# Kernel tuning notes

Hardware: AMD Instinct MI355X
Metric: run time of the kernel (lower is better)

Reference implementation:

```python
import jax, jax.numpy as jnp
import numpy as np

N_NODES = 50000
NEG_SLOPE = 0.2


def setup_inputs() -> dict:
    key = jax.random.key(0)
    ks = jax.random.split(key, 10)
    d = {
        'x': jax.random.normal(ks[0], (N_NODES, 128), dtype=jnp.float32),
        'edge_index': jax.random.randint(ks[1], (2, 800000), 0, N_NODES, dtype=jnp.int64),
        'W1': jax.random.normal(ks[2], (128, 512), dtype=jnp.float32) * (1.0 / np.sqrt(128)),
        'att_src1': jax.random.normal(ks[3], (8, 64), dtype=jnp.float32) * 0.1,
        'att_dst1': jax.random.normal(ks[4], (8, 64), dtype=jnp.float32) * 0.1,
        'b1': jax.random.normal(ks[5], (512,), dtype=jnp.float32) * 0.02,
        'W2': jax.random.normal(ks[6], (512, 1), dtype=jnp.float32) * (1.0 / np.sqrt(512)),
        'att_src2': jax.random.normal(ks[7], (1, 1), dtype=jnp.float32) * 0.1,
        'att_dst2': jax.random.normal(ks[8], (1, 1), dtype=jnp.float32) * 0.1,
        'b2': jax.random.normal(ks[9], (1,), dtype=jnp.float32) * 0.02,
    }
    return d


def _gat_layer(x, src, dst, W, a_src, a_dst, b):
    # x: [N, F_in]; W: [F_in, H*C]; a_src/a_dst: [H, C]; b: [H*C]
    N = x.shape[0]
    H, C = a_src.shape
    xh = (x @ W).reshape(N, H, C)                      # [N, H, C]
    s = jnp.sum(xh * a_src, axis=-1)                   # [N, H] source logits
    t = jnp.sum(xh * a_dst, axis=-1)                   # [N, H] target logits
    e = s[src] + t[dst]                                # [E, H]
    e = jnp.where(e > 0, e, NEG_SLOPE * e)             # leaky_relu(0.2)
    emax = jax.ops.segment_max(e, dst, num_segments=N)  # per-target max (self-loops guarantee coverage)
    ex = jnp.exp(e - emax[dst])                        # [E, H]
    denom = jax.ops.segment_sum(ex, dst, num_segments=N)  # [N, H]
    alpha = ex / denom[dst]                            # softmax over incoming edges
    msg = xh[src] * alpha[:, :, None]                  # [E, H, C]
    out = jax.ops.segment_sum(msg, dst, num_segments=N)   # [N, H, C]
    return out.reshape(N, H * C) + b


def reference(x, edge_index, W1, att_src1, att_dst1, b1, W2, att_src2, att_dst2, b2):
    N = x.shape[0]
    # add self-loops (PyG GATConv default)
    loop = jnp.arange(N, dtype=edge_index.dtype)
    src = jnp.concatenate([edge_index[0], loop])
    dst = jnp.concatenate([edge_index[1], loop])
    h = _gat_layer(x, src, dst, W1, att_src1, att_dst1, b1)   # [N, 512]
    h = jax.nn.relu(h)
    out = _gat_layer(h, src, dst, W2, att_src2, att_dst2, b2)  # [N, 1]
    return out.reshape(-1)
```

## Files before the change

### kernel.cpp

```cpp
#include <hip/hip_runtime.h>
#include <math.h>

#define NEG_SLOPE 0.2f

typedef __attribute__((ext_vector_type(8))) short bf16x8;
typedef __attribute__((ext_vector_type(4))) float f32x4;

__device__ __forceinline__ float leaky(float v){ return v > 0.f ? v : NEG_SLOPE * v; }

static __device__ __forceinline__ unsigned int f2bf(float x){
  unsigned u = __float_as_uint(x);
  return (u + 0x7fffu + ((u >> 16) & 1u)) >> 16;
}

__global__ __launch_bounds__(256) void k_prep0(
    const float* __restrict__ W1, const float* __restrict__ as, const float* __restrict__ ad,
    float* __restrict__ wst, bf16x8* __restrict__ packh,
    const int* __restrict__ dstp, int* __restrict__ deg8, int* __restrict__ erk,
    int N, int E)
{
  int b = blockIdx.x, tid = threadIdx.x;
  if (b == 0){
    for (int idx = tid; idx < 2048; idx += 256){
      int k = idx >> 4, o = idx & 15, half = o >> 3, hh = o & 7;
      const float* a = half ? ad : as;
      const float* wrow = W1 + (size_t)k * 512 + hh * 64;
      float sum = 0.f;
      for (int c = 0; c < 64; ++c) sum += wrow[c] * a[hh * 64 + c];
      wst[idx] = sum;
    }
  } else if (b < 33){
    int g = (b - 1) * 256 + tid;
    int gl = g & 63, kt = (g >> 6) & 3, ctl = (g >> 8) & 3, hh = g >> 10;
    int gc = hh * 64 + ctl * 16 + (gl & 15);
    int k0 = kt * 32 + (gl >> 4) * 8;
    bf16x8 hv;
    #pragma unroll
    for (int i = 0; i < 8; ++i)
      hv[i] = (short)f2bf(W1[(size_t)(k0 + i) * 512 + gc]);
    packh[g] = hv;
  } else {
    int i = (b - 33) * 256 + tid;
    if (i < E){
      int d = dstp[i];
      int s = b & 7;
      erk[i] = atomicAdd(&deg8[(size_t)s * N + d], 1);
    }
  }
}

__global__ __launch_bounds__(256) void k_scanlog(
    const int* __restrict__ deg8, int* __restrict__ sbase,
    int* __restrict__ tmp, int* __restrict__ bsum,
    const float* __restrict__ x, const float* __restrict__ wst,
    float* __restrict__ s, float* __restrict__ t, unsigned int* __restrict__ xb,
    int N, int nb)
{
  __shared__ float xs[64][133];
  __shared__ float wl[2048];
  __shared__ int ws4[4];
  int tid = threadIdx.x;
  int b = blockIdx.x;

  if (b < nb){
    int i = b * 256 + tid;
    int total = 0;
    if (i < N){
      int run = 0;
      #pragma unroll
      for (int sh = 0; sh < 8; ++sh){
        sbase[(size_t)sh * N + i] = run;
        run += deg8[(size_t)sh * N + i];
      }
      total = run;
    }
    int lane = tid & 63, wv = tid >> 6;
    int xv = total;
    #pragma unroll
    for (int off = 1; off < 64; off <<= 1){
      int y = __shfl_up(xv, off, 64);
      if (lane >= off) xv += y;
    }
    if (lane == 63) ws4[wv] = xv;
    __syncthreads();
    int p = 0;
    for (int w = 0; w < wv; ++w) p += ws4[w];
    xv += p;
    if (i < N) tmp[i] = xv;
    if (tid == 255) bsum[b] = xv;
  } else {
    int n0 = (b - nb) * 64;
    for (int i = tid; i < 2048; i += 256) wl[i] = wst[i];
    for (int i = tid; i < 2048; i += 256){
      int r = i >> 5, c4 = (i & 31) << 2;
      float4 v = make_float4(0.f, 0.f, 0.f, 0.f);
      if (n0 + r < N) v = *(const float4*)(x + (size_t)(n0 + r) * 128 + c4);
      xs[r][c4 + 0] = v.x; xs[r][c4 + 1] = v.y; xs[r][c4 + 2] = v.z; xs[r][c4 + 3] = v.w;
    }
    __syncthreads();
    int node = tid & 63, og = tid >> 6;
    int o = og * 4;
    float a0 = 0.f, a1 = 0.f, a2 = 0.f, a3 = 0.f;
    for (int k = 0; k < 128; ++k){
      float v = xs[node][k];
      float4 wv4 = *(const float4*)&wl[k * 16 + o];
      a0 += v * wv4.x;
      a1 += v * wv4.y;
      a2 += v * wv4.z;
      a3 += v * wv4.w;
    }
    int n = n0 + node;
    if (n < N){
      if (o < 8){
        s[n * 8 + o + 0] = a0; s[n * 8 + o + 1] = a1;
        s[n * 8 + o + 2] = a2; s[n * 8 + o + 3] = a3;
      } else {
        int oo = o - 8;
        t[n * 8 + oo + 0] = a0; t[n * 8 + oo + 1] = a1;
        t[n * 8 + oo + 2] = a2; t[n * 8 + oo + 3] = a3;
      }
    }
    for (int i = tid; i < 4096; i += 256){
      int r = i >> 6, j = i & 63;
      int n2 = n0 + r;
      if (n2 < N)
        xb[(size_t)n2 * 64 + j] = f2bf(xs[r][2 * j]) | (f2bf(xs[r][2 * j + 1]) << 16);
    }
  }
}

__global__ __launch_bounds__(256) void k_fill3(const int* __restrict__ src,
                        const int* __restrict__ dst, int E,
                        const int* __restrict__ tmp, const int* __restrict__ bsumraw,
                        const int* __restrict__ erk, const int* __restrict__ sbase,
                        int* __restrict__ rowptr, int* __restrict__ esrc, int N, int nb){
  __shared__ int bs[256];
  __shared__ int ws[4];
  int tid = threadIdx.x;
  {
    int v = (tid < nb) ? bsumraw[tid] : 0;
    int lane = tid & 63, wv = tid >> 6;
    int x = v;
    #pragma unroll
    for (int off = 1; off < 64; off <<= 1){
      int y = __shfl_up(x, off, 64);
      if (lane >= off) x += y;
    }
    if (lane == 63) ws[wv] = x;
    __syncthreads();
    int p = 0;
    for (int w = 0; w < wv; ++w) p += ws[w];
    bs[tid] = x + p;
    __syncthreads();
  }
  int i = blockIdx.x * 256 + tid;
  if (i <= N){
    int r;
    if (i == 0) r = 0;
    else { int ii = i - 1, blk = ii >> 8; r = tmp[ii] + (blk ? bs[blk - 1] : 0); }
    rowptr[i] = r;
  }
  if (i < E){
    int d = dst[i];
    int ii = d - 1, blk = ii >> 8;
    int row0 = (d == 0) ? 0 : tmp[ii] + (blk ? bs[blk - 1] : 0);
    int s = (33 + (i >> 8)) & 7;
    esrc[row0 + sbase[(size_t)s * N + d] + erk[i]] = src[i];
  }
}

__global__ __launch_bounds__(512, 8) void k_agg_gemm(
    const unsigned int* __restrict__ xb,
    const float* __restrict__ s, const float* __restrict__ t,
    const int* __restrict__ rowptr, const int* __restrict__ esrc,
    const bf16x8* __restrict__ packh,
    const float* __restrict__ b1, const float* __restrict__ W2,
    float* __restrict__ xh2, int N)
{
  __shared__ unsigned int ylds[8192];
  __shared__ float lal[8][128];
  __shared__ float red[8][16];
  int tid = threadIdx.x;
  int w = tid >> 6, lane = tid & 63;
  int m0 = blockIdx.x * 16;
  int h = lane & 7;
  int es = lane >> 3;

  for (int ni = 0; ni < 2; ++ni){
    int nl = w * 2 + ni;
    int n = m0 + nl;
    float acc[16];
    #pragma unroll
    for (int i = 0; i < 16; ++i) acc[i] = 0.f;

    if (n < N){
      int row0 = rowptr[n], deg = rowptr[n + 1] - row0;
      float tn = t[(unsigned)(n * 8 + h)];
      float sn = s[(unsigned)(n * 8 + h)];
      float selfe = __expf(leaky(sn + tn));

      {
        unsigned int v = xb[(unsigned)(n * 64 + lane)];
        float f0 = __uint_as_float(v << 16);
        float f1 = __uint_as_float(v & 0xffff0000u);
        #pragma unroll
        for (int hh = 0; hh < 8; ++hh){
          float a = __shfl(selfe, hh, 64);
          acc[2 * hh]     += a * f0;
          acc[2 * hh + 1] += a * f1;
        }
      }
      float dsum = (lane < 8) ? selfe : 0.f;

      float* lb = lal[w];
      for (int base = 0; base < deg; base += 8){
        float* la = lb + ((base >> 3) & 1) * 64;
        int e = base + es;
        int cnt = min(8, deg - base);
        int srcl = 0;
        if (e < deg) srcl = esrc[row0 + e];
        float sv = s[(unsigned)(srcl * 8 + h)];
        int sj[8];
        #pragma unroll
        for (int j = 0; j < 8; ++j) sj[j] = __shfl(srcl, j << 3, 64);
        unsigned int vv[8];
        #pragma unroll
        for (int j = 0; j < 8; ++j) vv[j] = xb[(unsigned)(sj[j] * 64 + lane)];
        float ev = (e < deg) ? __expf(leaky(sv + tn)) : 0.f;
        dsum += ev;
        la[lane] = ev;
        #pragma unroll
        for (int j = 0; j < 8; ++j){
          if (j < cnt){
            float4 q0 = *(float4*)&la[j * 8];
            float4 q1 = *(float4*)&la[j * 8 + 4];
            float f0 = __uint_as_float(vv[j] << 16);
            float f1 = __uint_as_float(vv[j] & 0xffff0000u);
            acc[0]  += q0.x * f0; acc[1]  += q0.x * f1;
            acc[2]  += q0.y * f0; acc[3]  += q0.y * f1;
            acc[4]  += q0.z * f0; acc[5]  += q0.z * f1;
            acc[6]  += q0.w * f0; acc[7]  += q0.w * f1;
            acc[8]  += q1.x * f0; acc[9]  += q1.x * f1;
            acc[10] += q1.y * f0; acc[11] += q1.y * f1;
            acc[12] += q1.z * f0; acc[13] += q1.z * f1;
            acc[14] += q1.w * f0; acc[15] += q1.w * f1;
          }
        }
      }

      dsum += __shfl_xor(dsum, 8, 64);
      dsum += __shfl_xor(dsum, 16, 64);
      dsum += __shfl_xor(dsum, 32, 64);
      float iden = 1.f / dsum;
      #pragma unroll
      for (int hh = 0; hh < 8; ++hh){
        float a = __shfl(iden, hh, 64);
        acc[2 * hh]     *= a;
        acc[2 * hh + 1] *= a;
      }
    }

    #pragma unroll
    for (int hh = 0; hh < 8; ++hh){
      unsigned int p = f2bf(acc[2 * hh]) | (f2bf(acc[2 * hh + 1]) << 16);
      unsigned int byte = (unsigned)(nl * 2048 + hh * 256 + lane * 4);
      byte ^= (unsigned)((nl & 7) << 4);
      ylds[byte >> 2] = p;
    }
  }
  __syncthreads();

  int lr = lane & 15, lg = lane >> 4;
  int hD = w;
  float pnode[4] = {0.f, 0.f, 0.f, 0.f};
  bf16x8 A[4];
  #pragma unroll
  for (int kt = 0; kt < 4; ++kt){
    unsigned int byte = (unsigned)(lr * 2048 + hD * 256 + kt * 64 + lg * 16);
    byte ^= (unsigned)((lr & 7) << 4);
    A[kt] = *(const bf16x8*)((const char*)ylds + byte);
  }
  #pragma unroll
  for (int ctl = 0; ctl < 4; ++ctl){
    f32x4 acc2 = {0.f, 0.f, 0.f, 0.f};
    int pb = ((hD * 4 + ctl) * 4) * 64 + lane;
    #pragma unroll
    for (int kt = 0; kt < 4; ++kt)
      acc2 = __builtin_amdgcn_mfma_f32_16x16x32_bf16(A[kt], packh[pb + kt * 64], acc2, 0, 0, 0);
    int gc = hD * 64 + ctl * 16 + lr;
    float bb = b1[gc], wvv = W2[gc];
    #pragma unroll
    for (int r = 0; r < 4; ++r){
      float o = acc2[r] + bb; o = o > 0.f ? o : 0.f;
      pnode[r] += o * wvv;
    }
  }
  #pragma unroll
  for (int r = 0; r < 4; ++r){
    float v = pnode[r];
    v += __shfl_xor(v, 1, 64);
    v += __shfl_xor(v, 2, 64);
    v += __shfl_xor(v, 4, 64);
    v += __shfl_xor(v, 8, 64);
    pnode[r] = v;
  }
  if (lr == 0){
    #pragma unroll
    for (int r = 0; r < 4; ++r) red[w][lg * 4 + r] = pnode[r];
  }
  __syncthreads();
  if (tid < 16){
    int node = m0 + tid;
    if (node < N){
      float sum = 0.f;
      #pragma unroll
      for (int ww = 0; ww < 8; ++ww) sum += red[ww][tid];
      xh2[node] = sum;
    }
  }
}

__global__ __launch_bounds__(256) void k_agg2(const float* __restrict__ xh2,
                       const int* __restrict__ rowptr, const int* __restrict__ esrc,
                       const float* __restrict__ as2p, const float* __restrict__ ad2p,
                       const float* __restrict__ b2p,
                       float* __restrict__ out, int N)
{
  int g = blockIdx.x * 32 + (threadIdx.x >> 3);
  int li = threadIdx.x & 7;
  if (g >= N) return;
  float a_s = as2p[0], a_d = ad2p[0], b2 = b2p[0];
  float xn = xh2[g];
  float t2 = a_d * xn;
  float den = 0.f, num = 0.f;
  if (li == 0){
    float w0 = __expf(leaky(a_s * xn + t2));
    den = w0; num = w0 * xn;
  }
  int row1 = rowptr[g + 1];
  for (int e = rowptr[g] + li; e < row1; e += 8){
    int src = esrc[e];
    float xs2 = xh2[src];
    float w = __expf(leaky(a_s * xs2 + t2));
    den += w; num += w * xs2;
  }
  den += __shfl_xor(den, 1, 64); num += __shfl_xor(num, 1, 64);
  den += __shfl_xor(den, 2, 64); num += __shfl_xor(num, 2, 64);
  den += __shfl_xor(den, 4, 64); num += __shfl_xor(num, 4, 64);
  if (li == 0) out[g] = num / den + b2;
}

extern "C" void kernel_launch(void* const* d_in, const int* in_sizes, int n_in,
                              void* d_out, int out_size, void* d_ws, size_t ws_size,
                              hipStream_t stream) {
  const float* x   = (const float*)d_in[0];
  const int*   ei  = (const int*)d_in[1];
  const float* W1  = (const float*)d_in[2];
  const float* as1 = (const float*)d_in[3];
  const float* ad1 = (const float*)d_in[4];
  const float* b1  = (const float*)d_in[5];
  const float* W2  = (const float*)d_in[6];
  const float* as2 = (const float*)d_in[7];
  const float* ad2 = (const float*)d_in[8];
  const float* b2  = (const float*)d_in[9];
  float* out = (float*)d_out;

  int N = in_sizes[0] / 128;
  int E = in_sizes[1] / 2;
  const int* src_in = ei;
  const int* dst_in = ei + E;

  char* w = (char*)d_ws;
  auto alloc = [&](size_t bytes){ void* p = (void*)w; w += (bytes + 255) & ~(size_t)255; return p; };
  unsigned int* xb   = (unsigned int*)alloc((size_t)N * 64 * 4);
  float* s      = (float*)alloc((size_t)N * 8 * 4);
  float* t      = (float*)alloc((size_t)N * 8 * 4);
  float* xh2    = (float*)alloc((size_t)N * 4);
  int*   deg8   = (int*)alloc((size_t)8 * N * 4);
  int*   sbase  = (int*)alloc((size_t)8 * N * 4);
  int*   rowptr = (int*)alloc((size_t)(N + 1) * 4);
  int*   esrc   = (int*)alloc((size_t)E * 4);
  int*   erk    = (int*)alloc((size_t)E * 4);
  int*   tmp    = (int*)alloc((size_t)N * 4);
  int*   bsum   = (int*)alloc((size_t)1024 * 4);
  float* wst    = (float*)alloc((size_t)2048 * 4);
  bf16x8* packh = (bf16x8*)alloc((size_t)8192 * 16);

  int nb     = (N + 255) / 256;
  int nhist  = (E + 255) / 256;
  int ntiles = (N + 63) / 64;

  hipMemsetAsync(deg8, 0, (size_t)8 * N * 4, stream);
  k_prep0<<<33 + nhist, 256, 0, stream>>>(W1, as1, ad1, wst, packh, dst_in, deg8, erk, N, E);
  k_scanlog<<<nb + ntiles, 256, 0, stream>>>(deg8, sbase, tmp, bsum, x, wst, s, t, xb, N, nb);
  k_fill3<<<(E + 255) / 256, 256, 0, stream>>>(src_in, dst_in, E, tmp, bsum, erk, sbase,
                                               rowptr, esrc, N, nb);
  k_agg_gemm<<<(N + 15) / 16, 512, 0, stream>>>(xb, s, t, rowptr, esrc, packh, b1, W2, xh2, N);
  k_agg2<<<(N + 31) / 32, 256, 0, stream>>>(xh2, rowptr, esrc, as2, ad2, b2, out, N);
}
```

Measured before the change: 170.5 us.

## Move logit/bf16 pack work from scan kernel into CSR fill kernel; vectorize accumulators

The per-node logit computation and bf16 packing of x move out of the scan kernel and into the CSR fill kernel. The scan becomes a small standalone kernel, and the fill and projection work share one launch, with the projection tile shrunk from 64 to 32 nodes. The aggregation kernel's accumulators become float2 vectors, so the compiler can emit packed FMAs, and the per-edge count guard is removed, relying on the zero attention weights of padded edges. The aim is to balance work across launches and cut ALU instructions, at the cost of more projection blocks that each reload W into LDS.

```diff
diff --git a/kernel.cpp b/kernel.cpp
--- a/kernel.cpp
+++ b/kernel.cpp
@@ -5,6 +5,7 @@
 
 typedef __attribute__((ext_vector_type(8))) short bf16x8;
 typedef __attribute__((ext_vector_type(4))) float f32x4;
+typedef __attribute__((ext_vector_type(2))) float f32x2;
 
 __device__ __forceinline__ float leaky(float v){ return v > 0.f ? v : NEG_SLOPE * v; }
 
@@ -49,123 +50,114 @@
   }
 }
 
-__global__ __launch_bounds__(256) void k_scanlog(
-    const int* __restrict__ deg8, int* __restrict__ sbase,
-    int* __restrict__ tmp, int* __restrict__ bsum,
+__global__ void k_scan1(const int* __restrict__ deg8, int* __restrict__ sbase,
+                        int* __restrict__ tmp, int* __restrict__ bsum, int N){
+  __shared__ int ws[4];
+  int tid = threadIdx.x;
+  int i = blockIdx.x * 256 + tid;
+  int total = 0;
+  if (i < N){
+    int run = 0;
+    #pragma unroll
+    for (int s = 0; s < 8; ++s){
+      sbase[(size_t)s * N + i] = run;
+      run += deg8[(size_t)s * N + i];
+    }
+    total = run;
+  }
+  int lane = tid & 63, wv = tid >> 6;
+  int x = total;
+  #pragma unroll
+  for (int off = 1; off < 64; off <<= 1){
+    int y = __shfl_up(x, off, 64);
+    if (lane >= off) x += y;
+  }
+  if (lane == 63) ws[wv] = x;
+  __syncthreads();
+  int p = 0;
+  for (int w = 0; w < wv; ++w) p += ws[w];
+  x += p;
+  if (i < N) tmp[i] = x;
+  if (tid == 255) bsum[blockIdx.x] = x;
+}
+
+__global__ __launch_bounds__(256) void k_fill_log(
+    const int* __restrict__ src, const int* __restrict__ dst, int E,
+    const int* __restrict__ tmp, const int* __restrict__ bsumraw,
+    const int* __restrict__ erk, const int* __restrict__ sbase,
+    int* __restrict__ rowptr, int* __restrict__ esrc,
     const float* __restrict__ x, const float* __restrict__ wst,
     float* __restrict__ s, float* __restrict__ t, unsigned int* __restrict__ xb,
-    int N, int nb)
+    int N, int nb, int nfill)
 {
-  __shared__ float xs[64][133];
+  __shared__ float xs[32][133];
   __shared__ float wl[2048];
   __shared__ int ws4[4];
   int tid = threadIdx.x;
   int b = blockIdx.x;
 
-  if (b < nb){
+  if (b < nfill){
+    int* bs = (int*)xs;
+    {
+      int v = (tid < nb) ? bsumraw[tid] : 0;
+      int lane = tid & 63, wv = tid >> 6;
+      int xv = v;
+      #pragma unroll
+      for (int off = 1; off < 64; off <<= 1){
+        int y = __shfl_up(xv, off, 64);
+        if (lane >= off) xv += y;
+      }
+      if (lane == 63) ws4[wv] = xv;
+      __syncthreads();
+      int p = 0;
+      for (int w = 0; w < wv; ++w) p += ws4[w];
+      bs[tid] = xv + p;
+      __syncthreads();
+    }
     int i = b * 256 + tid;
-    int total = 0;
-    if (i < N){
-      int run = 0;
-      #pragma unroll
-      for (int sh = 0; sh < 8; ++sh){
-        sbase[(size_t)sh * N + i] = run;
-        run += deg8[(size_t)sh * N + i];
-      }
-      total = run;
-    }
-    int lane = tid & 63, wv = tid >> 6;
-    int xv = total;
-    #pragma unroll
-    for (int off = 1; off < 64; off <<= 1){
-      int y = __shfl_up(xv, off, 64);
-      if (lane >= off) xv += y;
-    }
-    if (lane == 63) ws4[wv] = xv;
-    __syncthreads();
-    int p = 0;
-    for (int w = 0; w < wv; ++w) p += ws4[w];
-    xv += p;
-    if (i < N) tmp[i] = xv;
-    if (tid == 255) bsum[b] = xv;
+    if (i <= N){
+      int r;
+      if (i == 0) r = 0;
+      else { int ii = i - 1, blk = ii >> 8; r = tmp[ii] + (blk ? bs[blk - 1] : 0); }
+      rowptr[i] = r;
+    }
+    if (i < E){
+      int d = dst[i];
+      int ii = d - 1, blk = ii >> 8;
+      int row0 = (d == 0) ? 0 : tmp[ii] + (blk ? bs[blk - 1] : 0);
+      int sh = (33 + (i >> 8)) & 7;
+      esrc[row0 + sbase[(size_t)sh * N + d] + erk[i]] = src[i];
+    }
   } else {
-    int n0 = (b - nb) * 64;
+    int n0 = (b - nfill) * 32;
     for (int i = tid; i < 2048; i += 256) wl[i] = wst[i];
-    for (int i = tid; i < 2048; i += 256){
+    for (int i = tid; i < 1024; i += 256){
       int r = i >> 5, c4 = (i & 31) << 2;
       float4 v = make_float4(0.f, 0.f, 0.f, 0.f);
       if (n0 + r < N) v = *(const float4*)(x + (size_t)(n0 + r) * 128 + c4);
       xs[r][c4 + 0] = v.x; xs[r][c4 + 1] = v.y; xs[r][c4 + 2] = v.z; xs[r][c4 + 3] = v.w;
     }
     __syncthreads();
-    int node = tid & 63, og = tid >> 6;
-    int o = og * 4;
-    float a0 = 0.f, a1 = 0.f, a2 = 0.f, a3 = 0.f;
+    int node = tid & 31, og = tid >> 5;
+    int o = og * 2;
+    float a0 = 0.f, a1 = 0.f;
     for (int k = 0; k < 128; ++k){
       float v = xs[node][k];
-      float4 wv4 = *(const float4*)&wl[k * 16 + o];
-      a0 += v * wv4.x;
-      a1 += v * wv4.y;
-      a2 += v * wv4.z;
-      a3 += v * wv4.w;
+      float2 w2 = *(const float2*)&wl[k * 16 + o];
+      a0 += v * w2.x;
+      a1 += v * w2.y;
     }
     int n = n0 + node;
     if (n < N){
-      if (o < 8){
-        s[n * 8 + o + 0] = a0; s[n * 8 + o + 1] = a1;
-        s[n * 8 + o + 2] = a2; s[n * 8 + o + 3] = a3;
-      } else {
-        int oo = o - 8;
-        t[n * 8 + oo + 0] = a0; t[n * 8 + oo + 1] = a1;
-        t[n * 8 + oo + 2] = a2; t[n * 8 + oo + 3] = a3;
-      }
-    }
-    for (int i = tid; i < 4096; i += 256){
+      if (o < 8){ s[n * 8 + o] = a0; s[n * 8 + o + 1] = a1; }
+      else      { t[n * 8 + o - 8] = a0; t[n * 8 + o - 7] = a1; }
+    }
+    for (int i = tid; i < 2048; i += 256){
       int r = i >> 6, j = i & 63;
       int n2 = n0 + r;
       if (n2 < N)
         xb[(size_t)n2 * 64 + j] = f2bf(xs[r][2 * j]) | (f2bf(xs[r][2 * j + 1]) << 16);
     }
-  }
-}
-
-__global__ __launch_bounds__(256) void k_fill3(const int* __restrict__ src,
-                        const int* __restrict__ dst, int E,
-                        const int* __restrict__ tmp, const int* __restrict__ bsumraw,
-                        const int* __restrict__ erk, const int* __restrict__ sbase,
-                        int* __restrict__ rowptr, int* __restrict__ esrc, int N, int nb){
-  __shared__ int bs[256];
-  __shared__ int ws[4];
-  int tid = threadIdx.x;
-  {
-    int v = (tid < nb) ? bsumraw[tid] : 0;
-    int lane = tid & 63, wv = tid >> 6;
-    int x = v;
-    #pragma unroll
-    for (int off = 1; off < 64; off <<= 1){
-      int y = __shfl_up(x, off, 64);
-      if (lane >= off) x += y;
-    }
-    if (lane == 63) ws[wv] = x;
-    __syncthreads();
-    int p = 0;
-    for (int w = 0; w < wv; ++w) p += ws[w];
-    bs[tid] = x + p;
-    __syncthreads();
-  }
-  int i = blockIdx.x * 256 + tid;
-  if (i <= N){
-    int r;
-    if (i == 0) r = 0;
-    else { int ii = i - 1, blk = ii >> 8; r = tmp[ii] + (blk ? bs[blk - 1] : 0); }
-    rowptr[i] = r;
-  }
-  if (i < E){
-    int d = dst[i];
-    int ii = d - 1, blk = ii >> 8;
-    int row0 = (d == 0) ? 0 : tmp[ii] + (blk ? bs[blk - 1] : 0);
-    int s = (33 + (i >> 8)) & 7;
-    esrc[row0 + sbase[(size_t)s * N + d] + erk[i]] = src[i];
   }
 }
 
@@ -189,9 +181,9 @@
   for (int ni = 0; ni < 2; ++ni){
     int nl = w * 2 + ni;
     int n = m0 + nl;
-    float acc[16];
-    #pragma unroll
-    for (int i = 0; i < 16; ++i) acc[i] = 0.f;
+    f32x2 accv[8];
+    #pragma unroll
+    for (int i = 0; i < 8; ++i){ accv[i][0] = 0.f; accv[i][1] = 0.f; }
 
     if (n < N){
       int row0 = rowptr[n], deg = rowptr[n + 1] - row0;
@@ -201,13 +193,13 @@
 
       {
         unsigned int v = xb[(unsigned)(n * 64 + lane)];
-        float f0 = __uint_as_float(v << 16);
-        float f1 = __uint_as_float(v & 0xffff0000u);
+        f32x2 fp;
+        fp[0] = __uint_as_float(v << 16);
+        fp[1] = __uint_as_float(v & 0xffff0000u);
         #pragma unroll
         for (int hh = 0; hh < 8; ++hh){
           float a = __shfl(selfe, hh, 64);
-          acc[2 * hh]     += a * f0;
-          acc[2 * hh + 1] += a * f1;
+          accv[hh] += a * fp;
         }
       }
       float dsum = (lane < 8) ? selfe : 0.f;
@@ -216,7 +208,6 @@
       for (int base = 0; base < deg; base += 8){
         float* la = lb + ((base >> 3) & 1) * 64;
         int e = base + es;
-        int cnt = min(8, deg - base);
         int srcl = 0;
         if (e < deg) srcl = esrc[row0 + e];
         float sv = s[(unsigned)(srcl * 8 + h)];
@@ -231,20 +222,20 @@
         la[lane] = ev;
         #pragma unroll
         for (int j = 0; j < 8; ++j){
-          if (j < cnt){
-            float4 q0 = *(float4*)&la[j * 8];
-            float4 q1 = *(float4*)&la[j * 8 + 4];
-            float f0 = __uint_as_float(vv[j] << 16);
-            float f1 = __uint_as_float(vv[j] & 0xffff0000u);
-            acc[0]  += q0.x * f0; acc[1]  += q0.x * f1;
-            acc[2]  += q0.y * f0; acc[3]  += q0.y * f1;
-            acc[4]  += q0.z * f0; acc[5]  += q0.z * f1;
-            acc[6]  += q0.w * f0; acc[7]  += q0.w * f1;
-            acc[8]  += q1.x * f0; acc[9]  += q1.x * f1;
-            acc[10] += q1.y * f0; acc[11] += q1.y * f1;
-            acc[12] += q1.z * f0; acc[13] += q1.z * f1;
-            acc[14] += q1.w * f0; acc[15] += q1.w * f1;
-          }
+          float4 q0 = *(float4*)&la[j * 8];
+          float4 q1 = *(float4*)&la[j * 8 + 4];
+          unsigned int vj = vv[j];
+          f32x2 fp;
+          fp[0] = __uint_as_float(vj << 16);
+          fp[1] = __uint_as_float(vj & 0xffff0000u);
+          accv[0] += q0.x * fp;
+          accv[1] += q0.y * fp;
+          accv[2] += q0.z * fp;
+          accv[3] += q0.w * fp;
+          accv[4] += q1.x * fp;
+          accv[5] += q1.y * fp;
+          accv[6] += q1.z * fp;
+          accv[7] += q1.w * fp;
         }
       }
 
@@ -255,14 +246,13 @@
       #pragma unroll
       for (int hh = 0; hh < 8; ++hh){
         float a = __shfl(iden, hh, 64);
-        acc[2 * hh]     *= a;
-        acc[2 * hh + 1] *= a;
+        accv[hh] *= a;
       }
     }
 
     #pragma unroll
     for (int hh = 0; hh < 8; ++hh){
-      unsigned int p = f2bf(acc[2 * hh]) | (f2bf(acc[2 * hh + 1]) << 16);
+      unsigned int p = f2bf(accv[hh][0]) | (f2bf(accv[hh][1]) << 16);
       unsigned int byte = (unsigned)(nl * 2048 + hh * 256 + lane * 4);
       byte ^= (unsigned)((nl & 7) << 4);
       ylds[byte >> 2] = p;
@@ -386,15 +376,16 @@
   float* wst    = (float*)alloc((size_t)2048 * 4);
   bf16x8* packh = (bf16x8*)alloc((size_t)8192 * 16);
 
-  int nb     = (N + 255) / 256;
-  int nhist  = (E + 255) / 256;
-  int ntiles = (N + 63) / 64;
+  int nb      = (N + 255) / 256;
+  int nhist   = (E + 255) / 256;
+  int nfill   = (E + 255) / 256;
+  int ntiles  = (N + 31) / 32;
 
   hipMemsetAsync(deg8, 0, (size_t)8 * N * 4, stream);
   k_prep0<<<33 + nhist, 256, 0, stream>>>(W1, as1, ad1, wst, packh, dst_in, deg8, erk, N, E);
-  k_scanlog<<<nb + ntiles, 256, 0, stream>>>(deg8, sbase, tmp, bsum, x, wst, s, t, xb, N, nb);
-  k_fill3<<<(E + 255) / 256, 256, 0, stream>>>(src_in, dst_in, E, tmp, bsum, erk, sbase,
-                                               rowptr, esrc, N, nb);
+  k_scan1<<<nb, 256, 0, stream>>>(deg8, sbase, tmp, bsum, N);
+  k_fill_log<<<nfill + ntiles, 256, 0, stream>>>(src_in, dst_in, E, tmp, bsum, erk, sbase,
+                                                 rowptr, esrc, x, wst, s, t, xb, N, nb, nfill);
   k_agg_gemm<<<(N + 15) / 16, 512, 0, stream>>>(xb, s, t, rowptr, esrc, packh, b1, W2, xh2, N);
   k_agg2<<<(N + 31) / 32, 256, 0, stream>>>(xh2, rowptr, esrc, as2, ad2, b2, out, N);
 }
```

New measurement: 171.4 us. About the same (+0.5%).
